# Kernel optimization log

Hardware: AMD Instinct MI355X
Metric: run time of the kernel (lower is better)

## Reference

```python
import jax, jax.numpy as jnp
import numpy as np

T, B, IN_DIM, H = 512, 64, 1024, 1024

def setup_inputs() -> dict:
    key = jax.random.key(0)
    kx, kwx, kwh = jax.random.split(key, 3)
    x = jax.random.normal(kx, (T, B, IN_DIM), dtype=jnp.float32)
    # lecun_normal: std = 1/sqrt(fan_in)
    W_x = jax.random.normal(kwx, (IN_DIM, 4 * H), dtype=jnp.float32) / np.sqrt(IN_DIM)
    W_h = jax.random.normal(kwh, (H, 4 * H), dtype=jnp.float32) / np.sqrt(H)
    b = jnp.zeros((4 * H,), dtype=jnp.float32)
    return {"x": x, "W_x": W_x, "W_h": W_h, "b": b}

def reference(x, W_x, W_h, b):
    Tn, Bn, _ = x.shape
    Hn = W_h.shape[0]
    h0 = jnp.zeros((Bn, Hn), dtype=x.dtype)
    c0 = jnp.zeros((Bn, Hn), dtype=x.dtype)

    def step(carry, xt):
        h, c = carry
        gates = xt @ W_x + h @ W_h + b  # [B, 4H]
        i, f, g, o = jnp.split(gates, 4, axis=-1)
        i = jax.nn.sigmoid(i)
        f = jax.nn.sigmoid(f)
        o = jax.nn.sigmoid(o)
        g = jnp.tanh(g)
        c_new = f * c + i * g
        h_new = o * jnp.tanh(c_new)
        return (h_new, c_new), h_new

    (hT, cT), hs = jax.lax.scan(step, (h0, c0), x)
    return hs, (hT, cT)
```

## Files before the change

### kernel.cpp

```cpp
#include <hip/hip_runtime.h>

typedef unsigned short u16;
typedef unsigned int u32;
typedef unsigned long long u64;
typedef float f32x4 __attribute__((ext_vector_type(4)));
typedef __bf16 bf16x8 __attribute__((ext_vector_type(8)));
typedef u16 u16x8 __attribute__((ext_vector_type(8)));
typedef u32 u32x4 __attribute__((ext_vector_type(4)));

#define T_STEPS 512
#define BATCH 64
#define HDIM 1024
#define GDIM 4096
#define HS_ELEMS (33554432u)
#define XP_STEP 262144

__device__ __forceinline__ u16 f2bf(float f) {
  union { float f; u32 u; } v; v.f = f;
  u32 r = v.u + 0x7fffu + ((v.u >> 16) & 1u);
  return (u16)(r >> 16);
}
__device__ __forceinline__ float bf2f(u16 b) {
  union { u32 u; float f; } v; v.u = ((u32)b) << 16;
  return v.f;
}
__device__ __forceinline__ float sigm(float x) { return 1.f / (1.f + __expf(-x)); }
__device__ __forceinline__ float tanh_fast(float x) { return 1.f - 2.f / (__expf(2.f * x) + 1.f); }

__device__ __forceinline__ void gload16(const void* g, void* l) {
  __builtin_amdgcn_global_load_lds(
      (const __attribute__((address_space(1))) u32*)g,
      (__attribute__((address_space(3))) u32*)l, 16, 0, 0);
}
__device__ __forceinline__ u32x4 cload16(const void* g) {
  u32x4 r;
  asm volatile("global_load_dwordx4 %0, %1, off sc0 sc1" : "=&v"(r) : "v"(g) : "memory");
  return r;
}

__global__ void transpose_w(const float* __restrict__ Wx, const float* __restrict__ Wh,
                            u16* __restrict__ WxT, u16* __restrict__ WhT) {
  __shared__ float tile[32][33];
  const float* src = blockIdx.z ? Wh : Wx;
  u16* dst = blockIdx.z ? WhT : WxT;
  const int n0 = blockIdx.x * 32, k0 = blockIdx.y * 32;
  const int tx = threadIdx.x, ty = threadIdx.y;
#pragma unroll
  for (int i = 0; i < 4; ++i)
    tile[ty + i * 8][tx] = src[(size_t)(k0 + ty + i * 8) * GDIM + n0 + tx];
  __syncthreads();
#pragma unroll
  for (int i = 0; i < 4; ++i)
    dst[(size_t)(n0 + ty + i * 8) * HDIM + k0 + tx] = f2bf(tile[tx][ty + i * 8]);
}

__global__ void convert_x(const float* __restrict__ X, u16* __restrict__ Xbf) {
  const size_t i = ((size_t)blockIdx.x * 256 + threadIdx.x) * 8;
  const float4 a = *(const float4*)&X[i];
  const float4 b = *(const float4*)&X[i + 4];
  u16x8 o;
  o[0] = f2bf(a.x); o[1] = f2bf(a.y); o[2] = f2bf(a.z); o[3] = f2bf(a.w);
  o[4] = f2bf(b.x); o[5] = f2bf(b.y); o[6] = f2bf(b.z); o[7] = f2bf(b.w);
  *(u16x8*)&Xbf[i] = o;
}

__global__ __launch_bounds__(256) void gemm_xp(
    const u16* __restrict__ Xbf, const u16* __restrict__ WxT,
    const float* __restrict__ bias, u16* __restrict__ Xp) {
  __shared__ u16 As[128 * 32];
  __shared__ u16 Bs[128 * 32];
  const int tid = threadIdx.x;
  const int lane = tid & 63, w = tid >> 6;
  const int rl = lane & 15, gq = lane >> 4, g8 = gq * 8;
  const int swz = (blockIdx.x & 7) * 1024 + (blockIdx.x >> 3);
  const int m0 = (swz >> 5) * 128, n0 = (swz & 31) * 128;
  const int rbase = (w >> 1) * 64, cbase = (w & 1) * 64;
  const int r0 = tid >> 2, c0 = (tid & 3) * 8;

  f32x4 acc[4][4] = {};
  for (int k0 = 0; k0 < 1024; k0 += 32) {
    gload16(&Xbf[(size_t)(m0 + r0) * 1024 + k0 + c0], &As[w * 512]);
    gload16(&Xbf[(size_t)(m0 + r0 + 64) * 1024 + k0 + c0], &As[2048 + w * 512]);
    gload16(&WxT[(size_t)(n0 + r0) * 1024 + k0 + c0], &Bs[w * 512]);
    gload16(&WxT[(size_t)(n0 + r0 + 64) * 1024 + k0 + c0], &Bs[2048 + w * 512]);
    __syncthreads();
    bf16x8 av[4], bv[4];
#pragma unroll
    for (int i = 0; i < 4; ++i)
      av[i] = *(const bf16x8*)&As[(rbase + i * 16 + rl) * 32 + g8];
#pragma unroll
    for (int j = 0; j < 4; ++j)
      bv[j] = *(const bf16x8*)&Bs[(cbase + j * 16 + rl) * 32 + g8];
#pragma unroll
    for (int i = 0; i < 4; ++i)
#pragma unroll
      for (int j = 0; j < 4; ++j)
        acc[i][j] = __builtin_amdgcn_mfma_f32_16x16x32_bf16(av[i], bv[j], acc[i][j], 0, 0, 0);
    __syncthreads();
  }
#pragma unroll
  for (int j = 0; j < 4; ++j) {
    const int n = n0 + cbase + j * 16 + rl;
    const float bj = bias[n];
    const int gate = n >> 10, col = n & 1023;
    const int cri = col >> 5, hcoli = col & 31;
#pragma unroll
    for (int i = 0; i < 4; ++i)
#pragma unroll
      for (int r = 0; r < 4; ++r) {
        const int m = m0 + rbase + i * 16 + gq * 4 + r;
        const int tt = m >> 6, b = m & 63;
        Xp[(size_t)tt * XP_STEP + (size_t)((b >> 4) * 32 + cri) * 2048 +
           gate * 512 + (b & 15) * 32 + hcoli] = f2bf(acc[i][j][r] + bj);
      }
  }
}

__global__ void zero_tags(u32* __restrict__ ht) {
  const u32 i = blockIdx.x * 256 + threadIdx.x;
  if (i < 131200u) ht[i] = 0;
}

__global__ __launch_bounds__(512, 1) void lstm_rec(
    const u16* __restrict__ Xp, const u16* __restrict__ WhT,
    u32* __restrict__ h_tag, u32* __restrict__ flags, float* __restrict__ out) {
  __shared__ u16 h_lds[16 * 1024];
  __shared__ float gate_lds[4][2][16][20];
  const int tid = threadIdx.x;
  const int lane = tid & 63, w = tid >> 6;
  const int rl = lane & 15, gq = lane >> 4;
  const int cr = blockIdx.x & 31, bg = blockIdx.x >> 5;
  const int g = w >> 1, c2 = w & 1;

  bf16x8 wf[32];
  {
    const size_t gcol = (size_t)(g * 1024 + cr * 32 + c2 * 16 + rl) * HDIM + gq * 8;
#pragma unroll
    for (int kk = 0; kk < 32; ++kk)
      wf[kk] = *(const bf16x8*)&WhT[gcol + kk * 32];
  }

  const int b_el = tid >> 5, hcol = tid & 31;
  const int srow = tid >> 5, s32 = tid & 31;
  const int swz_w = ((srow & 7) << 4) ^ ((srow & 1) << 6);
  const int swz_r = ((rl & 7) << 4) ^ ((rl & 1) << 6);
  float creg = 0.f, hreg = 0.f;

  const u16* xp_p = Xp + (size_t)blockIdx.x * 2048 + tid;
  float xg0 = bf2f(xp_p[0]), xg1 = bf2f(xp_p[512]),
        xg2 = bf2f(xp_p[1024]), xg3 = bf2f(xp_p[1536]);

  const u32* flagrow = flags + bg * 32 + (lane & 31);

  for (int t = 0; t < T_STEPS; ++t) {
    u16 nx0 = 0, nx1 = 0, nx2 = 0, nx3 = 0;
    if (t + 1 < T_STEPS) {
      const u16* p = xp_p + XP_STEP;
      nx0 = p[0]; nx1 = p[512]; nx2 = p[1024]; nx3 = p[1536];
    }

    f32x4 acc0 = {0.f, 0.f, 0.f, 0.f}, acc1 = {0.f, 0.f, 0.f, 0.f};
    if (t > 0) {
      for (;;) {
        u32 f = __hip_atomic_load(flagrow, __ATOMIC_RELAXED, __HIP_MEMORY_SCOPE_AGENT);
        if (__all((int)(f >= (u32)t))) break;
      }
      const u32* hrow32 =
          h_tag + (size_t)(t & 1) * 65536 + (size_t)(bg * 16 + srow) * 1024;
      char* ldsrow = (char*)h_lds + srow * 2048;
      u32x4 v[8];
#pragma unroll
      for (int u = 0; u < 8; ++u)
        v[u] = cload16((const char*)hrow32 + 512 * u + 16 * s32);
      asm volatile("s_waitcnt vmcnt(0)" ::: "memory");
      __builtin_amdgcn_sched_barrier(0);
      u32 pend = 0u;
#pragma unroll
      for (int u = 0; u < 8; ++u) {
        const u32 w0 = v[u][0], w1 = v[u][1], w2 = v[u][2], w3 = v[u][3];
        const u64 packs = (u64)((w0 & 0xffffu) | (w1 << 16)) |
                          ((u64)((w2 & 0xffffu) | (w3 << 16)) << 32);
        *(u64*)(ldsrow + ((256 * u + 8 * s32) ^ swz_w)) = packs;
        if ((w0 >> 16) < (u32)t || (w1 >> 16) < (u32)t ||
            (w2 >> 16) < (u32)t || (w3 >> 16) < (u32)t)
          pend |= (1u << u);
      }
      while (__builtin_expect(pend != 0u, 0)) {
        const int uu = __ffs(pend) - 1;
        const u64* h64 = (const u64*)hrow32;
        const int j0 = 64 * uu + 2 * s32;
        u64 a = __hip_atomic_load(&h64[j0], __ATOMIC_RELAXED, __HIP_MEMORY_SCOPE_AGENT);
        u64 b = __hip_atomic_load(&h64[j0 + 1], __ATOMIC_RELAXED, __HIP_MEMORY_SCOPE_AGENT);
        const u32 t0 = (u32)(a >> 16) & 0xffffu, t1 = (u32)(a >> 48);
        const u32 t2 = (u32)(b >> 16) & 0xffffu, t3 = (u32)(b >> 48);
        if (t0 >= (u32)t && t1 >= (u32)t && t2 >= (u32)t && t3 >= (u32)t) {
          const u64 packs =
              (u64)(((u32)a & 0xffffu) | (((u32)(a >> 32) & 0xffffu) << 16)) |
              ((u64)(((u32)b & 0xffffu) | (((u32)(b >> 32) & 0xffffu) << 16)) << 32);
          *(u64*)(ldsrow + ((256 * uu + 8 * s32) ^ swz_w)) = packs;
          pend &= pend - 1u;
        }
      }
      __syncthreads();
      const char* hrd = (const char*)h_lds + rl * 2048;
#pragma unroll
      for (int kk = 0; kk < 32; kk += 2) {
        bf16x8 a0 = *(const bf16x8*)(hrd + ((kk * 64 + gq * 16) ^ swz_r));
        bf16x8 a1 = *(const bf16x8*)(hrd + (((kk + 1) * 64 + gq * 16) ^ swz_r));
        acc0 = __builtin_amdgcn_mfma_f32_16x16x32_bf16(a0, wf[kk], acc0, 0, 0, 0);
        acc1 = __builtin_amdgcn_mfma_f32_16x16x32_bf16(a1, wf[kk + 1], acc1, 0, 0, 0);
      }
      acc0 += acc1;
    } else {
      __syncthreads();
    }
#pragma unroll
    for (int r = 0; r < 4; ++r)
      gate_lds[g][c2][gq * 4 + r][rl] = acc0[r];
    __syncthreads();
    {
      const int cq = hcol >> 4, cl = hcol & 15;
      const float gi = gate_lds[0][cq][b_el][cl] + xg0;
      const float gf = gate_lds[1][cq][b_el][cl] + xg1;
      const float gg = gate_lds[2][cq][b_el][cl] + xg2;
      const float go = gate_lds[3][cq][b_el][cl] + xg3;
      const float iv = sigm(gi);
      const float fv = sigm(gf);
      const float gv = tanh_fast(gg);
      const float ov = sigm(go);
      creg = fv * creg + iv * gv;
      hreg = ov * tanh_fast(creg);
      const u32 wv = (u32)f2bf(hreg) | ((u32)(t + 1) << 16);
      __hip_atomic_store(
          &h_tag[(size_t)((t + 1) & 1) * 65536 + (size_t)(bg * 16 + b_el) * 1024 + cr * 32 + hcol],
          wv, __ATOMIC_RELAXED, __HIP_MEMORY_SCOPE_AGENT);
    }
    if (tid == 0)
      __hip_atomic_store(&flags[bg * 32 + cr], (u32)(t + 1), __ATOMIC_RELAXED,
                         __HIP_MEMORY_SCOPE_AGENT);
    out[((size_t)t * BATCH + bg * 16 + b_el) * HDIM + cr * 32 + hcol] = hreg;
    xg0 = bf2f(nx0); xg1 = bf2f(nx1); xg2 = bf2f(nx2); xg3 = bf2f(nx3);
    xp_p += XP_STEP;
  }
  out[(size_t)HS_ELEMS + (size_t)(bg * 16 + b_el) * HDIM + cr * 32 + hcol] = hreg;
  out[(size_t)HS_ELEMS + 65536u + (size_t)(bg * 16 + b_el) * HDIM + cr * 32 + hcol] = creg;
}

extern "C" void kernel_launch(void* const* d_in, const int* in_sizes, int n_in,
                              void* d_out, int out_size, void* d_ws, size_t ws_size,
                              hipStream_t stream) {
  const float* x = (const float*)d_in[0];
  const float* Wx = (const float*)d_in[1];
  const float* Wh = (const float*)d_in[2];
  const float* bias = (const float*)d_in[3];
  float* out = (float*)d_out;
  char* ws = (char*)d_ws;

  u16* WxT = (u16*)(ws + 0);
  u32* h_tag = (u32*)(ws + 0);
  u32* flags = (u32*)(ws + 524288);
  u16* WhT = (u16*)(ws + 8388608);
  u16* Xp = (u16*)(ws + 16777216);
  u16* Xbf = (u16*)d_out;

  transpose_w<<<dim3(128, 32, 2), dim3(32, 8), 0, stream>>>(Wx, Wh, WxT, WhT);
  convert_x<<<dim3(16384), dim3(256), 0, stream>>>(x, Xbf);
  gemm_xp<<<dim3(8192), dim3(256), 0, stream>>>(Xbf, WxT, bias, Xp);
  zero_tags<<<dim3(514), dim3(256), 0, stream>>>(h_tag);
  lstm_rec<<<dim3(128), dim3(512), 0, stream>>>(Xp, WhT, h_tag, flags, out);
}
```

Before: 2.267 ms.

## Fuse input-projection GEMM and LSTM recurrence into one co-running kernel

Merges the input-projection GEMM and the recurrent LSTM kernel into a single launch. The first 128 blocks run the recurrence while the remaining blocks compute Xp tiles and bump per-timestep counters. The recurrent blocks poll those counters before reading Xp, so the sequential recurrence can start before the whole GEMM finishes. The GEMM tile is widened to 128x256 with 512 threads, and Xp is stored and loaded with coherent (sc0 sc1) accesses. This relies on the first-dispatched blocks staying resident and on enough workspace; otherwise it falls back to the old sequential order.

```diff
diff --git a/kernel.cpp b/kernel.cpp
--- a/kernel.cpp
+++ b/kernel.cpp
@@ -37,6 +37,14 @@
   asm volatile("global_load_dwordx4 %0, %1, off sc0 sc1" : "=&v"(r) : "v"(g) : "memory");
   return r;
 }
+__device__ __forceinline__ u32 cload_u16(const void* g) {
+  u32 r;
+  asm volatile("global_load_ushort %0, %1, off sc0 sc1" : "=&v"(r) : "v"(g) : "memory");
+  return r;
+}
+__device__ __forceinline__ void cstore_u16(void* g, u16 v) {
+  asm volatile("global_store_short %0, %1, off sc0 sc1" :: "v"(g), "v"((u32)v) : "memory");
+}
 
 __global__ void transpose_w(const float* __restrict__ Wx, const float* __restrict__ Wh,
                             u16* __restrict__ WxT, u16* __restrict__ WhT) {
@@ -54,7 +62,9 @@
     dst[(size_t)(n0 + ty + i * 8) * HDIM + k0 + tx] = f2bf(tile[tx][ty + i * 8]);
 }
 
-__global__ void convert_x(const float* __restrict__ X, u16* __restrict__ Xbf) {
+__global__ void convert_x(const float* __restrict__ X, u16* __restrict__ Xbf,
+                          u32* __restrict__ cnt) {
+  if (blockIdx.x == 0 && threadIdx.x < 512) cnt[threadIdx.x] = 0;
   const size_t i = ((size_t)blockIdx.x * 256 + threadIdx.x) * 8;
   const float4 a = *(const float4*)&X[i];
   const float4 b = *(const float4*)&X[i + 4];
@@ -64,77 +74,88 @@
   *(u16x8*)&Xbf[i] = o;
 }
 
-__global__ __launch_bounds__(256) void gemm_xp(
+__global__ void zero_tags(u32* __restrict__ ht, u32 bound) {
+  const u32 i = blockIdx.x * 256 + threadIdx.x;
+  if (i < bound) ht[i] = 0;
+}
+
+__global__ __launch_bounds__(512, 1) void mega(
     const u16* __restrict__ Xbf, const u16* __restrict__ WxT,
-    const float* __restrict__ bias, u16* __restrict__ Xp) {
-  __shared__ u16 As[128 * 32];
-  __shared__ u16 Bs[128 * 32];
+    const u16* __restrict__ WhT, const float* __restrict__ bias,
+    u16* __restrict__ Xp, u32* __restrict__ cnt, u32* __restrict__ h_tag,
+    u32* __restrict__ flags, float* __restrict__ out, int lstm_blocks) {
+  extern __shared__ char smem[];
   const int tid = threadIdx.x;
   const int lane = tid & 63, w = tid >> 6;
-  const int rl = lane & 15, gq = lane >> 4, g8 = gq * 8;
-  const int swz = (blockIdx.x & 7) * 1024 + (blockIdx.x >> 3);
-  const int m0 = (swz >> 5) * 128, n0 = (swz & 31) * 128;
-  const int rbase = (w >> 1) * 64, cbase = (w & 1) * 64;
-  const int r0 = tid >> 2, c0 = (tid & 3) * 8;
-
-  f32x4 acc[4][4] = {};
-  for (int k0 = 0; k0 < 1024; k0 += 32) {
-    gload16(&Xbf[(size_t)(m0 + r0) * 1024 + k0 + c0], &As[w * 512]);
-    gload16(&Xbf[(size_t)(m0 + r0 + 64) * 1024 + k0 + c0], &As[2048 + w * 512]);
-    gload16(&WxT[(size_t)(n0 + r0) * 1024 + k0 + c0], &Bs[w * 512]);
-    gload16(&WxT[(size_t)(n0 + r0 + 64) * 1024 + k0 + c0], &Bs[2048 + w * 512]);
+
+  if ((int)blockIdx.x >= lstm_blocks) {
+    const int gb = blockIdx.x - lstm_blocks;
+    const int swz = (gb & 7) * 512 + (gb >> 3);
+    const int m0 = (swz >> 4) * 128, n0 = (swz & 15) * 256;
+    const int gi = w >> 2, wg = w & 3;
+    const int rl = lane & 15, gq = lane >> 4, g8 = gq * 8;
+    const int rbase = (wg >> 1) * 64, cbase = (wg & 1) * 64;
+    u16* As = (u16*)smem;
+    u16* Bsg = (u16*)(smem + 8192 + gi * 8192);
+    const int c1 = wg * 64 + lane, c2 = c1 + 256;
+
+    f32x4 acc[4][4] = {};
+    for (int k0 = 0; k0 < 1024; k0 += 32) {
+      gload16(&Xbf[(size_t)(m0 + (tid >> 2)) * 1024 + k0 + (tid & 3) * 8], &As[w * 512]);
+      gload16(&WxT[(size_t)(n0 + gi * 128 + (c1 >> 2)) * 1024 + k0 + (c1 & 3) * 8],
+              &Bsg[wg * 512]);
+      gload16(&WxT[(size_t)(n0 + gi * 128 + (c2 >> 2)) * 1024 + k0 + (c2 & 3) * 8],
+              &Bsg[wg * 512 + 2048]);
+      __syncthreads();
+      bf16x8 av[4], bv[4];
+#pragma unroll
+      for (int i = 0; i < 4; ++i)
+        av[i] = *(const bf16x8*)&As[(rbase + i * 16 + rl) * 32 + g8];
+#pragma unroll
+      for (int j = 0; j < 4; ++j)
+        bv[j] = *(const bf16x8*)&Bsg[(cbase + j * 16 + rl) * 32 + g8];
+#pragma unroll
+      for (int i = 0; i < 4; ++i)
+#pragma unroll
+        for (int j = 0; j < 4; ++j)
+          acc[i][j] = __builtin_amdgcn_mfma_f32_16x16x32_bf16(av[i], bv[j], acc[i][j], 0, 0, 0);
+      __syncthreads();
+    }
+#pragma unroll
+    for (int j = 0; j < 4; ++j) {
+      const int n = n0 + gi * 128 + cbase + j * 16 + rl;
+      const float bj = bias[n];
+      const int gate = n >> 10, col = n & 1023;
+      const int cri = col >> 5, hcoli = col & 31;
+#pragma unroll
+      for (int i = 0; i < 4; ++i)
+#pragma unroll
+        for (int r = 0; r < 4; ++r) {
+          const int m = m0 + rbase + i * 16 + gq * 4 + r;
+          const int tt = m >> 6, b = m & 63;
+          cstore_u16(&Xp[(size_t)tt * XP_STEP + (size_t)((b >> 4) * 32 + cri) * 2048 +
+                         gate * 512 + (b & 15) * 32 + hcoli],
+                     f2bf(acc[i][j][r] + bj));
+        }
+    }
+    asm volatile("s_waitcnt vmcnt(0)" ::: "memory");
     __syncthreads();
-    bf16x8 av[4], bv[4];
-#pragma unroll
-    for (int i = 0; i < 4; ++i)
-      av[i] = *(const bf16x8*)&As[(rbase + i * 16 + rl) * 32 + g8];
-#pragma unroll
-    for (int j = 0; j < 4; ++j)
-      bv[j] = *(const bf16x8*)&Bs[(cbase + j * 16 + rl) * 32 + g8];
-#pragma unroll
-    for (int i = 0; i < 4; ++i)
-#pragma unroll
-      for (int j = 0; j < 4; ++j)
-        acc[i][j] = __builtin_amdgcn_mfma_f32_16x16x32_bf16(av[i], bv[j], acc[i][j], 0, 0, 0);
-    __syncthreads();
-  }
-#pragma unroll
-  for (int j = 0; j < 4; ++j) {
-    const int n = n0 + cbase + j * 16 + rl;
-    const float bj = bias[n];
-    const int gate = n >> 10, col = n & 1023;
-    const int cri = col >> 5, hcoli = col & 31;
-#pragma unroll
-    for (int i = 0; i < 4; ++i)
-#pragma unroll
-      for (int r = 0; r < 4; ++r) {
-        const int m = m0 + rbase + i * 16 + gq * 4 + r;
-        const int tt = m >> 6, b = m & 63;
-        Xp[(size_t)tt * XP_STEP + (size_t)((b >> 4) * 32 + cri) * 2048 +
-           gate * 512 + (b & 15) * 32 + hcoli] = f2bf(acc[i][j][r] + bj);
-      }
-  }
-}
-
-__global__ void zero_tags(u32* __restrict__ ht) {
-  const u32 i = blockIdx.x * 256 + threadIdx.x;
-  if (i < 131200u) ht[i] = 0;
-}
-
-__global__ __launch_bounds__(512, 1) void lstm_rec(
-    const u16* __restrict__ Xp, const u16* __restrict__ WhT,
-    u32* __restrict__ h_tag, u32* __restrict__ flags, float* __restrict__ out) {
-  __shared__ u16 h_lds[16 * 1024];
-  __shared__ float gate_lds[4][2][16][20];
-  const int tid = threadIdx.x;
-  const int lane = tid & 63, w = tid >> 6;
+    if (tid < 2)
+      __hip_atomic_fetch_add(&cnt[(m0 >> 6) + tid], 1u, __ATOMIC_RELAXED,
+                             __HIP_MEMORY_SCOPE_AGENT);
+    return;
+  }
+
+  u16* h_lds = (u16*)smem;
+  float* gate_f = (float*)(smem + 32768);
+#define GATE(g_, c_, r_, cc_) gate_f[(((g_)*2 + (c_)) * 16 + (r_)) * 20 + (cc_)]
   const int rl = lane & 15, gq = lane >> 4;
   const int cr = blockIdx.x & 31, bg = blockIdx.x >> 5;
-  const int g = w >> 1, c2 = w & 1;
+  const int g = w >> 1, c2w = w & 1;
 
   bf16x8 wf[32];
   {
-    const size_t gcol = (size_t)(g * 1024 + cr * 32 + c2 * 16 + rl) * HDIM + gq * 8;
+    const size_t gcol = (size_t)(g * 1024 + cr * 32 + c2w * 16 + rl) * HDIM + gq * 8;
 #pragma unroll
     for (int kk = 0; kk < 32; ++kk)
       wf[kk] = *(const bf16x8*)&WhT[gcol + kk * 32];
@@ -147,24 +168,46 @@
   float creg = 0.f, hreg = 0.f;
 
   const u16* xp_p = Xp + (size_t)blockIdx.x * 2048 + tid;
-  float xg0 = bf2f(xp_p[0]), xg1 = bf2f(xp_p[512]),
-        xg2 = bf2f(xp_p[1024]), xg3 = bf2f(xp_p[1536]);
-
-  const u32* flagrow = flags + bg * 32 + (lane & 31);
+
+  for (;;) {
+    u32 c = __hip_atomic_load(cnt, __ATOMIC_RELAXED, __HIP_MEMORY_SCOPE_AGENT);
+    if (__all((int)(c >= 16u))) break;
+  }
+  u32 cx0 = cload_u16(xp_p), cx1 = cload_u16(xp_p + 512),
+      cx2 = cload_u16(xp_p + 1024), cx3 = cload_u16(xp_p + 1536);
+  asm volatile("s_waitcnt vmcnt(0)" ::: "memory");
+  __builtin_amdgcn_sched_barrier(0);
+  float xg0 = bf2f((u16)cx0), xg1 = bf2f((u16)cx1),
+        xg2 = bf2f((u16)cx2), xg3 = bf2f((u16)cx3);
 
   for (int t = 0; t < T_STEPS; ++t) {
-    u16 nx0 = 0, nx1 = 0, nx2 = 0, nx3 = 0;
+    {
+      const u32* myaddr;
+      bool skip;
+      u32 thr;
+      if (lane < 32) {
+        myaddr = flags + bg * 32 + lane; skip = (t == 0); thr = (u32)t;
+      } else if (lane < 48) {
+        const int tn = (t + 1 < T_STEPS) ? t + 1 : 0;
+        myaddr = cnt + tn; skip = (t + 1 >= T_STEPS); thr = 16u;
+      } else {
+        const int tc = 2 * t - 512 + ((lane >> 3) & 1);
+        myaddr = cnt + ((t >= 256) ? tc : 0); skip = (t < 256); thr = 16u;
+      }
+      for (;;) {
+        u32 f = __hip_atomic_load(myaddr, __ATOMIC_RELAXED, __HIP_MEMORY_SCOPE_AGENT);
+        if (__all((int)(skip || f >= thr))) break;
+      }
+    }
+    u32 nx0 = 0, nx1 = 0, nx2 = 0, nx3 = 0;
     if (t + 1 < T_STEPS) {
       const u16* p = xp_p + XP_STEP;
-      nx0 = p[0]; nx1 = p[512]; nx2 = p[1024]; nx3 = p[1536];
+      nx0 = cload_u16(p); nx1 = cload_u16(p + 512);
+      nx2 = cload_u16(p + 1024); nx3 = cload_u16(p + 1536);
     }
 
     f32x4 acc0 = {0.f, 0.f, 0.f, 0.f}, acc1 = {0.f, 0.f, 0.f, 0.f};
     if (t > 0) {
-      for (;;) {
-        u32 f = __hip_atomic_load(flagrow, __ATOMIC_RELAXED, __HIP_MEMORY_SCOPE_AGENT);
-        if (__all((int)(f >= (u32)t))) break;
-      }
       const u32* hrow32 =
           h_tag + (size_t)(t & 1) * 65536 + (size_t)(bg * 16 + srow) * 1024;
       char* ldsrow = (char*)h_lds + srow * 2048;
@@ -213,17 +256,19 @@
       acc0 += acc1;
     } else {
       __syncthreads();
+      asm volatile("s_waitcnt vmcnt(0)" ::: "memory");
+      __builtin_amdgcn_sched_barrier(0);
     }
 #pragma unroll
     for (int r = 0; r < 4; ++r)
-      gate_lds[g][c2][gq * 4 + r][rl] = acc0[r];
+      GATE(g, c2w, gq * 4 + r, rl) = acc0[r];
     __syncthreads();
     {
       const int cq = hcol >> 4, cl = hcol & 15;
-      const float gi = gate_lds[0][cq][b_el][cl] + xg0;
-      const float gf = gate_lds[1][cq][b_el][cl] + xg1;
-      const float gg = gate_lds[2][cq][b_el][cl] + xg2;
-      const float go = gate_lds[3][cq][b_el][cl] + xg3;
+      const float gi = GATE(0, cq, b_el, cl) + xg0;
+      const float gf = GATE(1, cq, b_el, cl) + xg1;
+      const float gg = GATE(2, cq, b_el, cl) + xg2;
+      const float go = GATE(3, cq, b_el, cl) + xg3;
       const float iv = sigm(gi);
       const float fv = sigm(gf);
       const float gv = tanh_fast(gg);
@@ -239,11 +284,13 @@
       __hip_atomic_store(&flags[bg * 32 + cr], (u32)(t + 1), __ATOMIC_RELAXED,
                          __HIP_MEMORY_SCOPE_AGENT);
     out[((size_t)t * BATCH + bg * 16 + b_el) * HDIM + cr * 32 + hcol] = hreg;
-    xg0 = bf2f(nx0); xg1 = bf2f(nx1); xg2 = bf2f(nx2); xg3 = bf2f(nx3);
+    xg0 = bf2f((u16)nx0); xg1 = bf2f((u16)nx1);
+    xg2 = bf2f((u16)nx2); xg3 = bf2f((u16)nx3);
     xp_p += XP_STEP;
   }
   out[(size_t)HS_ELEMS + (size_t)(bg * 16 + b_el) * HDIM + cr * 32 + hcol] = hreg;
   out[(size_t)HS_ELEMS + 65536u + (size_t)(bg * 16 + b_el) * HDIM + cr * 32 + hcol] = creg;
+#undef GATE
 }
 
 extern "C" void kernel_launch(void* const* d_in, const int* in_sizes, int n_in,
@@ -257,15 +304,26 @@
   char* ws = (char*)d_ws;
 
   u16* WxT = (u16*)(ws + 0);
-  u32* h_tag = (u32*)(ws + 0);
-  u32* flags = (u32*)(ws + 524288);
   u16* WhT = (u16*)(ws + 8388608);
   u16* Xp = (u16*)(ws + 16777216);
-  u16* Xbf = (u16*)d_out;
+  u16* Xbf = (u16*)((char*)d_out + 67108864);
+
+  const bool corun = ws_size >= (size_t)285739520;
+  u32* h_tag = corun ? (u32*)(ws + 285212672) : (u32*)ws;
+  u32* flags = h_tag + 131072;
+  u32* cnt = corun ? (h_tag + 131200) : (u32*)((char*)d_out + 134217728);
 
   transpose_w<<<dim3(128, 32, 2), dim3(32, 8), 0, stream>>>(Wx, Wh, WxT, WhT);
-  convert_x<<<dim3(16384), dim3(256), 0, stream>>>(x, Xbf);
-  gemm_xp<<<dim3(8192), dim3(256), 0, stream>>>(Xbf, WxT, bias, Xp);
-  zero_tags<<<dim3(514), dim3(256), 0, stream>>>(h_tag);
-  lstm_rec<<<dim3(128), dim3(512), 0, stream>>>(Xp, WhT, h_tag, flags, out);
-}
+  convert_x<<<dim3(16384), dim3(256), 0, stream>>>(x, Xbf, cnt);
+  if (corun) {
+    zero_tags<<<dim3(515), dim3(256), 0, stream>>>(h_tag, 131712u);
+    mega<<<dim3(4224), dim3(512), 43008, stream>>>(Xbf, WxT, WhT, bias, Xp, cnt,
+                                                   h_tag, flags, out, 128);
+  } else {
+    mega<<<dim3(4096), dim3(512), 43008, stream>>>(Xbf, WxT, WhT, bias, Xp, cnt,
+                                                   h_tag, flags, out, 0);
+    zero_tags<<<dim3(513), dim3(256), 0, stream>>>(h_tag, 131200u);
+    mega<<<dim3(128), dim3(512), 43008, stream>>>(Xbf, WxT, WhT, bias, Xp, cnt,
+                                                  h_tag, flags, out, 128);
+  }
+}
```

New measurement: 2.934 ms. +29.4%, slower.

## Halve recurrent grid to 64 blocks, each computing 64 hidden columns

Applied to the files above, without the earlier changes.

The persistent recurrent kernel now runs 64 workgroups instead of 128. Each one owns 64 hidden columns per batch group and holds twice as many W_h fragments in registers (two sets of 32 bf16x8 vectors). This halves the number of producers each block must wait on per step (16 flags instead of 32), which cuts cross-block synchronisation traffic, at the cost of doubling per-block MFMA and gate work and raising register pressure. The Xp layout and the tag-zeroing range are adjusted to match, and the slow-path retry now uses a single 16-byte load instead of two 64-bit atomics.

```diff
diff --git a/kernel.cpp b/kernel.cpp
--- a/kernel.cpp
+++ b/kernel.cpp
@@ -103,67 +103,74 @@
     const int n = n0 + cbase + j * 16 + rl;
     const float bj = bias[n];
     const int gate = n >> 10, col = n & 1023;
-    const int cri = col >> 5, hcoli = col & 31;
+    const int cri = col >> 6, hcoli = col & 63;
 #pragma unroll
     for (int i = 0; i < 4; ++i)
 #pragma unroll
       for (int r = 0; r < 4; ++r) {
         const int m = m0 + rbase + i * 16 + gq * 4 + r;
         const int tt = m >> 6, b = m & 63;
-        Xp[(size_t)tt * XP_STEP + (size_t)((b >> 4) * 32 + cri) * 2048 +
-           gate * 512 + (b & 15) * 32 + hcoli] = f2bf(acc[i][j][r] + bj);
+        Xp[(size_t)tt * XP_STEP + (size_t)((b >> 4) * 16 + cri) * 4096 +
+           gate * 1024 + (b & 15) * 64 + hcoli] = f2bf(acc[i][j][r] + bj);
       }
   }
 }
 
 __global__ void zero_tags(u32* __restrict__ ht) {
   const u32 i = blockIdx.x * 256 + threadIdx.x;
-  if (i < 131200u) ht[i] = 0;
+  if (i < 131136u) ht[i] = 0;
 }
 
 __global__ __launch_bounds__(512, 1) void lstm_rec(
     const u16* __restrict__ Xp, const u16* __restrict__ WhT,
     u32* __restrict__ h_tag, u32* __restrict__ flags, float* __restrict__ out) {
   __shared__ u16 h_lds[16 * 1024];
-  __shared__ float gate_lds[4][2][16][20];
+  __shared__ float gate_lds[4][4][16][20];
   const int tid = threadIdx.x;
   const int lane = tid & 63, w = tid >> 6;
   const int rl = lane & 15, gq = lane >> 4;
-  const int cr = blockIdx.x & 31, bg = blockIdx.x >> 5;
+  const int cr = blockIdx.x & 15, bg = blockIdx.x >> 4;
   const int g = w >> 1, c2 = w & 1;
 
-  bf16x8 wf[32];
+  bf16x8 wf0[32], wf1[32];
   {
-    const size_t gcol = (size_t)(g * 1024 + cr * 32 + c2 * 16 + rl) * HDIM + gq * 8;
-#pragma unroll
-    for (int kk = 0; kk < 32; ++kk)
-      wf[kk] = *(const bf16x8*)&WhT[gcol + kk * 32];
-  }
-
-  const int b_el = tid >> 5, hcol = tid & 31;
+    const size_t gc0 = (size_t)(g * 1024 + cr * 64 + c2 * 32 + rl) * HDIM + gq * 8;
+    const size_t gc1 = gc0 + (size_t)16 * HDIM;
+#pragma unroll
+    for (int kk = 0; kk < 32; ++kk) {
+      wf0[kk] = *(const bf16x8*)&WhT[gc0 + kk * 32];
+      wf1[kk] = *(const bf16x8*)&WhT[gc1 + kk * 32];
+    }
+  }
+
+  const int b_el = tid >> 5, hc0 = tid & 31;
   const int srow = tid >> 5, s32 = tid & 31;
   const int swz_w = ((srow & 7) << 4) ^ ((srow & 1) << 6);
   const int swz_r = ((rl & 7) << 4) ^ ((rl & 1) << 6);
-  float creg = 0.f, hreg = 0.f;
-
-  const u16* xp_p = Xp + (size_t)blockIdx.x * 2048 + tid;
-  float xg0 = bf2f(xp_p[0]), xg1 = bf2f(xp_p[512]),
-        xg2 = bf2f(xp_p[1024]), xg3 = bf2f(xp_p[1536]);
-
-  const u32* flagrow = flags + bg * 32 + (lane & 31);
+  float cA = 0.f, hA = 0.f, cB = 0.f, hB = 0.f;
+
+  const u16* xp_p = Xp + (size_t)blockIdx.x * 4096 + b_el * 64 + hc0;
+  float xa0 = bf2f(xp_p[0]),    xa1 = bf2f(xp_p[1024]),
+        xa2 = bf2f(xp_p[2048]), xa3 = bf2f(xp_p[3072]);
+  float xb0 = bf2f(xp_p[32]),   xb1 = bf2f(xp_p[1056]),
+        xb2 = bf2f(xp_p[2080]), xb3 = bf2f(xp_p[3104]);
+
+  const u32* flagrow = flags + bg * 16 + (lane & 15);
 
   for (int t = 0; t < T_STEPS; ++t) {
-    u16 nx0 = 0, nx1 = 0, nx2 = 0, nx3 = 0;
+    u16 na0 = 0, na1 = 0, na2 = 0, na3 = 0, nb0 = 0, nb1 = 0, nb2 = 0, nb3 = 0;
     if (t + 1 < T_STEPS) {
       const u16* p = xp_p + XP_STEP;
-      nx0 = p[0]; nx1 = p[512]; nx2 = p[1024]; nx3 = p[1536];
-    }
-
-    f32x4 acc0 = {0.f, 0.f, 0.f, 0.f}, acc1 = {0.f, 0.f, 0.f, 0.f};
+      na0 = p[0];  na1 = p[1024]; na2 = p[2048]; na3 = p[3072];
+      nb0 = p[32]; nb1 = p[1056]; nb2 = p[2080]; nb3 = p[3104];
+    }
+
+    f32x4 aA0 = {0.f, 0.f, 0.f, 0.f}, aA1 = {0.f, 0.f, 0.f, 0.f};
+    f32x4 aB0 = {0.f, 0.f, 0.f, 0.f}, aB1 = {0.f, 0.f, 0.f, 0.f};
     if (t > 0) {
       for (;;) {
         u32 f = __hip_atomic_load(flagrow, __ATOMIC_RELAXED, __HIP_MEMORY_SCOPE_AGENT);
-        if (__all((int)(f >= (u32)t))) break;
+        if (__all((int)((lane >= 16) | (f >= (u32)t)))) break;
       }
       const u32* hrow32 =
           h_tag + (size_t)(t & 1) * 65536 + (size_t)(bg * 16 + srow) * 1024;
@@ -187,16 +194,13 @@
       }
       while (__builtin_expect(pend != 0u, 0)) {
         const int uu = __ffs(pend) - 1;
-        const u64* h64 = (const u64*)hrow32;
-        const int j0 = 64 * uu + 2 * s32;
-        u64 a = __hip_atomic_load(&h64[j0], __ATOMIC_RELAXED, __HIP_MEMORY_SCOPE_AGENT);
-        u64 b = __hip_atomic_load(&h64[j0 + 1], __ATOMIC_RELAXED, __HIP_MEMORY_SCOPE_AGENT);
-        const u32 t0 = (u32)(a >> 16) & 0xffffu, t1 = (u32)(a >> 48);
-        const u32 t2 = (u32)(b >> 16) & 0xffffu, t3 = (u32)(b >> 48);
-        if (t0 >= (u32)t && t1 >= (u32)t && t2 >= (u32)t && t3 >= (u32)t) {
-          const u64 packs =
-              (u64)(((u32)a & 0xffffu) | (((u32)(a >> 32) & 0xffffu) << 16)) |
-              ((u64)(((u32)b & 0xffffu) | (((u32)(b >> 32) & 0xffffu) << 16)) << 32);
+        u32x4 q = cload16((const char*)hrow32 + 512 * uu + 16 * s32);
+        asm volatile("s_waitcnt vmcnt(0)" ::: "memory");
+        const u32 w0 = q[0], w1 = q[1], w2 = q[2], w3 = q[3];
+        if ((w0 >> 16) >= (u32)t && (w1 >> 16) >= (u32)t &&
+            (w2 >> 16) >= (u32)t && (w3 >> 16) >= (u32)t) {
+          const u64 packs = (u64)((w0 & 0xffffu) | (w1 << 16)) |
+                            ((u64)((w2 & 0xffffu) | (w3 << 16)) << 32);
           *(u64*)(ldsrow + ((256 * uu + 8 * s32) ^ swz_w)) = packs;
           pend &= pend - 1u;
         }
@@ -207,43 +211,62 @@
       for (int kk = 0; kk < 32; kk += 2) {
         bf16x8 a0 = *(const bf16x8*)(hrd + ((kk * 64 + gq * 16) ^ swz_r));
         bf16x8 a1 = *(const bf16x8*)(hrd + (((kk + 1) * 64 + gq * 16) ^ swz_r));
-        acc0 = __builtin_amdgcn_mfma_f32_16x16x32_bf16(a0, wf[kk], acc0, 0, 0, 0);
-        acc1 = __builtin_amdgcn_mfma_f32_16x16x32_bf16(a1, wf[kk + 1], acc1, 0, 0, 0);
-      }
-      acc0 += acc1;
+        aA0 = __builtin_amdgcn_mfma_f32_16x16x32_bf16(a0, wf0[kk], aA0, 0, 0, 0);
+        aA1 = __builtin_amdgcn_mfma_f32_16x16x32_bf16(a1, wf0[kk + 1], aA1, 0, 0, 0);
+        aB0 = __builtin_amdgcn_mfma_f32_16x16x32_bf16(a0, wf1[kk], aB0, 0, 0, 0);
+        aB1 = __builtin_amdgcn_mfma_f32_16x16x32_bf16(a1, wf1[kk + 1], aB1, 0, 0, 0);
+      }
+      aA0 += aA1;
+      aB0 += aB1;
     } else {
       __syncthreads();
     }
 #pragma unroll
-    for (int r = 0; r < 4; ++r)
-      gate_lds[g][c2][gq * 4 + r][rl] = acc0[r];
+    for (int r = 0; r < 4; ++r) {
+      gate_lds[g][c2 * 2][gq * 4 + r][rl] = aA0[r];
+      gate_lds[g][c2 * 2 + 1][gq * 4 + r][rl] = aB0[r];
+    }
     __syncthreads();
     {
-      const int cq = hcol >> 4, cl = hcol & 15;
-      const float gi = gate_lds[0][cq][b_el][cl] + xg0;
-      const float gf = gate_lds[1][cq][b_el][cl] + xg1;
-      const float gg = gate_lds[2][cq][b_el][cl] + xg2;
-      const float go = gate_lds[3][cq][b_el][cl] + xg3;
-      const float iv = sigm(gi);
-      const float fv = sigm(gf);
-      const float gv = tanh_fast(gg);
-      const float ov = sigm(go);
-      creg = fv * creg + iv * gv;
-      hreg = ov * tanh_fast(creg);
-      const u32 wv = (u32)f2bf(hreg) | ((u32)(t + 1) << 16);
-      __hip_atomic_store(
-          &h_tag[(size_t)((t + 1) & 1) * 65536 + (size_t)(bg * 16 + b_el) * 1024 + cr * 32 + hcol],
-          wv, __ATOMIC_RELAXED, __HIP_MEMORY_SCOPE_AGENT);
+      const int q = hc0 >> 4, cl = hc0 & 15;
+      const float giA = gate_lds[0][q][b_el][cl] + xa0;
+      const float gfA = gate_lds[1][q][b_el][cl] + xa1;
+      const float ggA = gate_lds[2][q][b_el][cl] + xa2;
+      const float goA = gate_lds[3][q][b_el][cl] + xa3;
+      cA = sigm(gfA) * cA + sigm(giA) * tanh_fast(ggA);
+      hA = sigm(goA) * tanh_fast(cA);
+      const float giB = gate_lds[0][q + 2][b_el][cl] + xb0;
+      const float gfB = gate_lds[1][q + 2][b_el][cl] + xb1;
+      const float ggB = gate_lds[2][q + 2][b_el][cl] + xb2;
+      const float goB = gate_lds[3][q + 2][b_el][cl] + xb3;
+      cB = sigm(gfB) * cB + sigm(giB) * tanh_fast(ggB);
+      hB = sigm(goB) * tanh_fast(cB);
+      const size_t hb = (size_t)((t + 1) & 1) * 65536 +
+                        (size_t)(bg * 16 + b_el) * 1024 + cr * 64 + hc0;
+      __hip_atomic_store(&h_tag[hb], (u32)f2bf(hA) | ((u32)(t + 1) << 16),
+                         __ATOMIC_RELAXED, __HIP_MEMORY_SCOPE_AGENT);
+      __hip_atomic_store(&h_tag[hb + 32], (u32)f2bf(hB) | ((u32)(t + 1) << 16),
+                         __ATOMIC_RELAXED, __HIP_MEMORY_SCOPE_AGENT);
     }
     if (tid == 0)
-      __hip_atomic_store(&flags[bg * 32 + cr], (u32)(t + 1), __ATOMIC_RELAXED,
+      __hip_atomic_store(&flags[bg * 16 + cr], (u32)(t + 1), __ATOMIC_RELAXED,
                          __HIP_MEMORY_SCOPE_AGENT);
-    out[((size_t)t * BATCH + bg * 16 + b_el) * HDIM + cr * 32 + hcol] = hreg;
-    xg0 = bf2f(nx0); xg1 = bf2f(nx1); xg2 = bf2f(nx2); xg3 = bf2f(nx3);
+    {
+      const size_t ob = ((size_t)t * BATCH + bg * 16 + b_el) * HDIM + cr * 64 + hc0;
+      out[ob] = hA;
+      out[ob + 32] = hB;
+    }
+    xa0 = bf2f(na0); xa1 = bf2f(na1); xa2 = bf2f(na2); xa3 = bf2f(na3);
+    xb0 = bf2f(nb0); xb1 = bf2f(nb1); xb2 = bf2f(nb2); xb3 = bf2f(nb3);
     xp_p += XP_STEP;
   }
-  out[(size_t)HS_ELEMS + (size_t)(bg * 16 + b_el) * HDIM + cr * 32 + hcol] = hreg;
-  out[(size_t)HS_ELEMS + 65536u + (size_t)(bg * 16 + b_el) * HDIM + cr * 32 + hcol] = creg;
+  {
+    const size_t tb = (size_t)HS_ELEMS + (size_t)(bg * 16 + b_el) * HDIM + cr * 64 + hc0;
+    out[tb] = hA;
+    out[tb + 32] = hB;
+    out[tb + 65536u] = cA;
+    out[tb + 65536u + 32] = cB;
+  }
 }
 
 extern "C" void kernel_launch(void* const* d_in, const int* in_sizes, int n_in,
@@ -266,6 +289,6 @@
   transpose_w<<<dim3(128, 32, 2), dim3(32, 8), 0, stream>>>(Wx, Wh, WxT, WhT);
   convert_x<<<dim3(16384), dim3(256), 0, stream>>>(x, Xbf);
   gemm_xp<<<dim3(8192), dim3(256), 0, stream>>>(Xbf, WxT, bias, Xp);
-  zero_tags<<<dim3(514), dim3(256), 0, stream>>>(h_tag);
-  lstm_rec<<<dim3(128), dim3(512), 0, stream>>>(Xp, WhT, h_tag, flags, out);
-}
+  zero_tags<<<dim3(513), dim3(256), 0, stream>>>(h_tag);
+  lstm_rec<<<dim3(64), dim3(512), 0, stream>>>(Xp, WhT, h_tag, flags, out);
+}
```

After: 5.768 ms. +154.4%, slower.
